# Kernel optimization log

Measured on AMD Instinct MI355X. Metric: run time of the kernel, lower is better.

The kernel has to match this reference:

```python
import jax, jax.numpy as jnp
from jax import lax
import numpy as np

B, T, E, H, ENC, V = 64, 49, 512, 512, 1024, 32000


def setup_inputs() -> dict:
    key = jax.random.key(0)
    ks = jax.random.split(key, 12)
    embeddings = jax.random.normal(ks[0], (B, T, E), jnp.float32)
    encoder_out = jax.random.normal(ks[1], (B, ENC), jnp.float32)
    # caption lengths sorted descending (module assumes this for ragged truncation)
    lens = jax.random.randint(ks[2], (B,), 10, T + 2)
    caption_lengths = jnp.sort(lens)[::-1]
    caption_lengths = caption_lengths.at[0].set(T + 1)  # max decode length == T
    s = 1.0 / np.sqrt(H)
    u = lambda k, shp, lim: jax.random.uniform(k, shp, jnp.float32, -lim, lim)
    W_ih = u(ks[3], (4 * H, E), s)
    W_hh = u(ks[4], (4 * H, H), s)
    b_ih = u(ks[5], (4 * H,), s)
    b_hh = u(ks[6], (4 * H,), s)
    se = 1.0 / np.sqrt(ENC)
    W_init_h = u(ks[7], (H, ENC), se)
    b_init_h = u(ks[8], (H,), se)
    W_init_c = u(ks[9], (H, ENC), se)
    b_init_c = u(ks[10], (H,), se)
    W_fc = u(ks[11], (V, H), 0.1)  # init_weights: uniform(-0.1, 0.1)
    b_fc = jnp.zeros((V,), jnp.float32)
    return dict(embeddings=embeddings, encoder_out=encoder_out,
                caption_lengths=caption_lengths,
                W_ih=W_ih, W_hh=W_hh, b_ih=b_ih, b_hh=b_hh,
                W_init_h=W_init_h, b_init_h=b_init_h,
                W_init_c=W_init_c, b_init_c=b_init_c,
                W_fc=W_fc, b_fc=b_fc)


def reference(embeddings, encoder_out, caption_lengths,
              W_ih, W_hh, b_ih, b_hh,
              W_init_h, b_init_h, W_init_c, b_init_c,
              W_fc, b_fc):
    # dropout is treated as identity (eval mode) for the deterministic reference
    h0 = encoder_out @ W_init_h.T + b_init_h  # [B, H]
    c0 = encoder_out @ W_init_c.T + b_init_c
    decode_lengths = caption_lengths - 1
    Tn = embeddings.shape[1]
    # mask[t, b] = True iff example b is still active at step t
    mask = jnp.arange(Tn)[:, None] < decode_lengths[None, :]  # [T, B]
    xs = jnp.transpose(embeddings, (1, 0, 2))  # [T, B, E]

    def step(carry, inp):
        h, c = carry
        x, m = inp
        gates = x @ W_ih.T + b_ih + h @ W_hh.T + b_hh  # [B, 4H]
        i, f, g, o = jnp.split(gates, 4, axis=-1)
        i = jax.nn.sigmoid(i); f = jax.nn.sigmoid(f)
        g = jnp.tanh(g); o = jax.nn.sigmoid(o)
        c_new = f * c + i * g
        h_new = o * jnp.tanh(c_new)
        preds = h_new @ W_fc.T + b_fc  # [B, V]
        m2 = m[:, None]
        # inactive rows: state frozen (torch only updates h[:batch_size_t]),
        # predictions stay zero
        h = jnp.where(m2, h_new, h)
        c = jnp.where(m2, c_new, c)
        preds = jnp.where(m2, preds, 0.0)
        return (h, c), preds

    (_, _), preds = lax.scan(step, (h0, c0), (xs, mask))
    predictions = jnp.transpose(preds, (1, 0, 2))  # [B, T, V]
    return predictions, decode_lengths
```

## Files before the change

### kernel.cpp

```cpp
#include <hip/hip_runtime.h>
#include <stdint.h>

#define B_    64
#define T_    49
#define E_    512
#define H_    512
#define ENC_  1024
#define V_    32000
#define G4_   2048
#define M_    3136
#define MPAD_ 3200
#define NPROD 32
#define NWG   512
#define NTN   250

typedef __attribute__((ext_vector_type(8))) short bf16x8;
typedef __attribute__((ext_vector_type(4))) float f32x4;

static __device__ __forceinline__ unsigned short f2bf(float f) {
  union { float f; uint32_t u; } v; v.f = f;
  uint32_t r = v.u + 0x7FFFu + ((v.u >> 16) & 1u);
  return (unsigned short)(r >> 16);
}

static __device__ __forceinline__ void async16(const void* g, void* lds) {
  __builtin_amdgcn_global_load_lds(
      (const __attribute__((address_space(1))) unsigned int*)g,
      (__attribute__((address_space(3))) unsigned int*)lds, 16, 0, 0);
}

static __device__ __forceinline__ float sigf(float x) { return 1.0f / (1.0f + expf(-x)); }

__global__ __launch_bounds__(256) void convert_kernel(
    const float* __restrict__ Wih, const float* __restrict__ Whh,
    const float* __restrict__ Wfc, const float* __restrict__ emb,
    unsigned short* __restrict__ WihB, unsigned short* __restrict__ WhhB,
    unsigned short* __restrict__ WfcB, unsigned short* __restrict__ AxB) {
  const int n_wih = (G4_ * E_) / 4;
  const int n_whh = (G4_ * H_) / 4;
  const int n_wfc = (V_ * H_) / 4;
  const int n_emb = (B_ * T_ * E_) / 4;
  const int n_pad = ((MPAD_ - M_) * E_) / 4;
  const long total = (long)n_wih + n_whh + n_wfc + n_emb + n_pad;
  for (long u = (long)blockIdx.x * blockDim.x + threadIdx.x; u < total;
       u += (long)gridDim.x * blockDim.x) {
    long i = u;
    if (i < n_wih) {
      float4 v = ((const float4*)Wih)[i];
      ushort4 o; o.x = f2bf(v.x); o.y = f2bf(v.y); o.z = f2bf(v.z); o.w = f2bf(v.w);
      ((ushort4*)WihB)[i] = o; continue;
    }
    i -= n_wih;
    if (i < n_whh) {
      float4 v = ((const float4*)Whh)[i];
      ushort4 o; o.x = f2bf(v.x); o.y = f2bf(v.y); o.z = f2bf(v.z); o.w = f2bf(v.w);
      ((ushort4*)WhhB)[i] = o; continue;
    }
    i -= n_whh;
    if (i < n_wfc) {
      float4 v = ((const float4*)Wfc)[i];
      ushort4 o; o.x = f2bf(v.x); o.y = f2bf(v.y); o.z = f2bf(v.z); o.w = f2bf(v.w);
      ((ushort4*)WfcB)[i] = o; continue;
    }
    i -= n_wfc;
    if (i < n_emb) {
      int bt = (int)(i >> 7);
      int e4 = (int)(i & 127);
      int b = bt / T_, t = bt - b * T_;
      float4 v = ((const float4*)emb)[i];
      ushort4 o; o.x = f2bf(v.x); o.y = f2bf(v.y); o.z = f2bf(v.z); o.w = f2bf(v.w);
      ((ushort4*)AxB)[((long)(t * 64 + b) << 7) + e4] = o; continue;
    }
    i -= n_emb;
    ushort4 z; z.x = z.y = z.z = z.w = 0;
    ((ushort4*)AxB)[((long)M_ << 7) + i] = z;
  }
}

__global__ __launch_bounds__(256) void init_kernel(
    const float* __restrict__ enc, const int* __restrict__ cap,
    const float* __restrict__ Wh, const float* __restrict__ bh,
    const float* __restrict__ Wc, const float* __restrict__ bc,
    unsigned short* __restrict__ h0b, float* __restrict__ c0,
    float* __restrict__ out_dl, int* __restrict__ meta,
    int* __restrict__ rowmap, int* __restrict__ zrowmap) {
  __shared__ __align__(16) float e[ENC_];
  __shared__ int s_nb[T_];
  __shared__ int s_start[T_ + 1];
  const int b = blockIdx.x, q = blockIdx.y, tid = threadIdx.x;
  ((float4*)e)[tid] = ((const float4*)(enc + (size_t)b * ENC_))[tid];
  __syncthreads();
  const bool is_c = tid >= 128;
  const int j = q * 128 + (tid & 127);
  const float* W = is_c ? Wc : Wh;
  float s = is_c ? bc[j] : bh[j];
  const float4* wr = (const float4*)(W + (size_t)j * ENC_);
  const float4* e4 = (const float4*)e;
#pragma unroll 4
  for (int k = 0; k < ENC_ / 4; ++k) {
    float4 w = wr[k], v = e4[k];
    s += w.x * v.x + w.y * v.y + w.z * v.z + w.w * v.w;
  }
  if (is_c) c0[(size_t)b * H_ + j] = s;
  else      h0b[(size_t)b * H_ + j] = f2bf(s);
  if (b == 0 && q == 0 && tid < B_) out_dl[tid] = (float)(cap[tid] - 1);

  if (b == 0 && q == 0) {
    __syncthreads();
    if (tid < T_) {
      int cnt = 0;
      for (int bb = 0; bb < B_; ++bb) cnt += (cap[bb] - 1 > tid) ? 1 : 0;
      s_nb[tid] = cnt;
    }
    __syncthreads();
    if (tid == 0) {
      int acc = 0;
      for (int t = 0; t < T_; ++t) { s_start[t] = acc; acc += s_nb[t]; }
      s_start[T_] = acc;
      const int Mc = acc;
      const int MT = (Mc + 127) >> 7;
      meta[100] = Mc;
      meta[101] = MT;
      meta[102] = MT * NTN;
      meta[103] = M_ - Mc;
      meta[104] = M_ - Mc;
      meta[105] = (M_ - Mc) + MT * NTN;
      for (int i = Mc; i < MT * 128; ++i) rowmap[i] = -1;
    }
    __syncthreads();
    if (tid < T_) {
      meta[tid] = s_start[tid];
      const int st = s_start[tid], nb = s_nb[tid];
      for (int bb = 0; bb < nb; ++bb) rowmap[st + bb] = bb * T_ + tid;
      int zst = 0;
      for (int t2 = 0; t2 < tid; ++t2) zst += B_ - s_nb[t2];
      for (int bb = nb; bb < B_; ++bb) zrowmap[zst + (bb - nb)] = bb * T_ + tid;
    }
    __syncthreads();
    if (tid < 26) {
      const int Mc = s_start[T_];
      const int MT = (Mc + 127) >> 7;
      if (tid < MT) {
        int last = tid * 128 + 127;
        if (last > Mc - 1) last = Mc - 1;
        int tlast = 0;
        for (int t2 = 0; t2 < T_; ++t2) if (s_start[t2] <= last) tlast = t2;
        meta[110 + tid] = tlast + 1;
      }
    }
  }
}

__global__ __launch_bounds__(256) void pad_kernel(const int* __restrict__ meta,
                                                  unsigned short* __restrict__ Hall) {
  const int Mc = meta[100], MT = meta[101];
  const int tot = (MT * 128 - Mc) * 64;
  for (int i = blockIdx.x * blockDim.x + threadIdx.x; i < tot;
       i += gridDim.x * blockDim.x) {
    const int row = Mc + (i >> 6), c = i & 63;
    ushort4 z; z.x = z.y = z.z = z.w = 0;
    *(ushort4*)((char*)Hall + (size_t)row * 1024 + c * 16) = z;
  }
}

__global__ __launch_bounds__(256) void gemm_gx(
    const unsigned short* __restrict__ A, const unsigned short* __restrict__ Bm,
    float* __restrict__ C, const float* __restrict__ bias0, const float* __restrict__ bias1) {
  __shared__ __align__(16) char smem[65536];
  const int tid = threadIdx.x, lane = tid & 63, wid = tid >> 6;
  const int nt = blockIdx.x, mt = blockIdx.y;
  const int wr = wid >> 1, wc = wid & 1;
  const int m0 = mt * 128, n0 = nt * 128;
  f32x4 acc[4][4] = {};

  auto stage = [&](int buf, int kit) {
    const int k0b = kit * 128;
#pragma unroll
    for (int i = 0; i < 4; ++i) {
      int chunk = wid * 4 + i;
      int d = chunk * 1024 + lane * 16;
      int row = d >> 7, colb = d & 127;
      int sc = colb ^ ((row & 7) << 4);
      async16((const char*)A + (size_t)(m0 + row) * 1024 + k0b + sc,
              smem + buf * 16384 + chunk * 1024);
      async16((const char*)Bm + (size_t)(n0 + row) * 1024 + k0b + sc,
              smem + 32768 + buf * 16384 + chunk * 1024);
    }
  };

  stage(0, 0);
  __syncthreads();
  for (int kit = 0; kit < 8; ++kit) {
    const int buf = kit & 1;
    if (kit < 7) stage(buf ^ 1, kit + 1);
    const char* Ab = smem + buf * 16384;
    const char* Bb = smem + 32768 + buf * 16384;
#pragma unroll
    for (int kb = 0; kb < 2; ++kb) {
      const int colb = kb * 64 + (lane >> 4) * 16;
      bf16x8 af[4], bfb[4];
#pragma unroll
      for (int rt = 0; rt < 4; ++rt) {
        int ar = wr * 64 + rt * 16 + (lane & 15);
        af[rt] = *(const bf16x8*)(Ab + ar * 128 + (colb ^ ((ar & 7) << 4)));
        int br = wc * 64 + rt * 16 + (lane & 15);
        bfb[rt] = *(const bf16x8*)(Bb + br * 128 + (colb ^ ((br & 7) << 4)));
      }
#pragma unroll
      for (int i = 0; i < 4; ++i)
#pragma unroll
        for (int j = 0; j < 4; ++j)
          acc[i][j] = __builtin_amdgcn_mfma_f32_16x16x32_bf16(af[i], bfb[j], acc[i][j], 0, 0, 0);
    }
    __syncthreads();
  }
#pragma unroll
  for (int i = 0; i < 4; ++i) {
    const int rbase = m0 + wr * 64 + i * 16 + (lane >> 4) * 4;
#pragma unroll
    for (int j = 0; j < 4; ++j) {
      const int col = n0 + wc * 64 + j * 16 + (lane & 15);
#pragma unroll
      for (int r = 0; r < 4; ++r)
        C[(size_t)(rbase + r) * G4_ + col] = acc[i][j][r] + bias0[col] + bias1[col];
    }
  }
}

__global__ __launch_bounds__(256) void fused_kernel(
    const float* __restrict__ Gx, const unsigned short* __restrict__ WhhB,
    const unsigned short* __restrict__ h0b, const float* __restrict__ c0,
    unsigned short* __restrict__ hsl, unsigned short* __restrict__ Hall,
    const unsigned short* __restrict__ WfcB, const float* __restrict__ bfc,
    const int* __restrict__ cap, float* __restrict__ outp,
    int* __restrict__ ctrl, const int* __restrict__ meta,
    const int* __restrict__ rowmap, const int* __restrict__ zrowmap) {
  __shared__ __align__(16) char smem[81920];
  const int tid = threadIdx.x, lane = tid & 63, g = tid >> 6;
  int* s_tile = (int*)(smem + 81916);

  if (blockIdx.x < NPROD) {
    __builtin_amdgcn_s_setprio(1);
    const int w = blockIdx.x, hc0 = w * 16;
    const int gcol = g * 512 + hc0 + (lane & 15);
    const int ko = (lane >> 4) * 8;
    bf16x8 wf[16];
#pragma unroll
    for (int kb = 0; kb < 16; ++kb)
      wf[kb] = *(const bf16x8*)&WhhB[(size_t)gcol * 512 + kb * 32 + ko];
    const int b = tid >> 2, hq = (tid & 3) * 4, hc = hc0 + hq;
    const int dl = cap[b] - 1;
    f32x4 creg = *(const f32x4*)&c0[b * H_ + hc];
    ushort4 hold = *(const ushort4*)&h0b[b * H_ + hc];
    const int myoff = ((b * 32) ^ (((b >> 2) & 7) << 4) ^ ((hq >> 3) << 4)) + ((hq & 7) * 2);
    {
      union { ushort4 s; unsigned long long u; } cv; cv.s = hold;
      __hip_atomic_store((unsigned long long*)((char*)hsl + w * 2048 + myoff), cv.u,
                         __ATOMIC_RELAXED, __HIP_MEMORY_SCOPE_AGENT);
    }
    int arb[4];
#pragma unroll
    for (int rt = 0; rt < 4; ++rt) {
      int ar = rt * 16 + (lane & 15);
      arb[rt] = (ar * 32) ^ (((ar >> 2) & 7) << 4) ^ (((lane >> 4) & 1) << 4);
    }
    const int chunk_hi = lane >> 5;
    float (*gl)[64][16] = (float (*)[64][16])(smem + 65536);
    asm volatile("s_waitcnt vmcnt(0)" ::: "memory");
    __syncthreads();
    if (tid == 0)
      __hip_atomic_store(&ctrl[w * 16], 1, __ATOMIC_RELAXED, __HIP_MEMORY_SCOPE_AGENT);

    for (int t = 0; t < T_; ++t) {
      const size_t gxr = ((size_t)t * 64 + b) * (size_t)G4_ + hc;
      f32x4 xi = *(const f32x4*)&Gx[gxr + 0];
      f32x4 xf = *(const f32x4*)&Gx[gxr + 512];
      f32x4 xg = *(const f32x4*)&Gx[gxr + 1024];
      f32x4 xo = *(const f32x4*)&Gx[gxr + 1536];
      __builtin_amdgcn_sched_barrier(0);
      if (tid < 64) {
        const int need = t + 1;
        for (;;) {
          int v = (lane < NPROD)
                      ? __hip_atomic_load(&ctrl[lane * 16], __ATOMIC_RELAXED, __HIP_MEMORY_SCOPE_AGENT)
                      : need;
          if (__all(v >= need)) break;
          __builtin_amdgcn_s_sleep(1);
        }
        if (tid == 0 && w == 0 && t > 0)
          __hip_atomic_store(&ctrl[512], t, __ATOMIC_RELAXED, __HIP_MEMORY_SCOPE_AGENT);
      }
      __syncthreads();
      {
        const char* src = (const char*)hsl + (t & 1) * 65536 + g * 16384 + lane * 8;
        char* dst = smem + g * 16384 + lane * 8;
        unsigned long long hv[32];
#pragma unroll
        for (int i = 0; i < 32; ++i)
          hv[i] = __hip_atomic_load((const unsigned long long*)(src + i * 512),
                                    __ATOMIC_RELAXED, __HIP_MEMORY_SCOPE_AGENT);
#pragma unroll
        for (int i = 0; i < 32; ++i)
          *(unsigned long long*)(dst + i * 512) = hv[i];
      }
      __syncthreads();
      f32x4 accp[4] = {};
#pragma unroll
      for (int kb = 0; kb < 16; ++kb) {
        const int cbase = (kb * 2 + chunk_hi) * 2048;
#pragma unroll
        for (int rt = 0; rt < 4; ++rt) {
          bf16x8 af = *(const bf16x8*)(smem + cbase + arb[rt]);
          accp[rt] = __builtin_amdgcn_mfma_f32_16x16x32_bf16(af, wf[kb], accp[rt], 0, 0, 0);
        }
      }
#pragma unroll
      for (int rt = 0; rt < 4; ++rt)
#pragma unroll
        for (int r = 0; r < 4; ++r)
          gl[g][rt * 16 + (lane >> 4) * 4 + r][lane & 15] = accp[rt][r];
      __syncthreads();
      f32x4 vi = xi + *(const f32x4*)&gl[0][b][hq];
      f32x4 vf = xf + *(const f32x4*)&gl[1][b][hq];
      f32x4 vg = xg + *(const f32x4*)&gl[2][b][hq];
      f32x4 vo = xo + *(const f32x4*)&gl[3][b][hq];
      f32x4 cn;
      ushort4 hb16;
      {
        float hv[4];
#pragma unroll
        for (int k = 0; k < 4; ++k) {
          float iv = sigf(vi[k]), fv = sigf(vf[k]), gv = tanhf(vg[k]), ov = sigf(vo[k]);
          cn[k] = fv * creg[k] + iv * gv;
          hv[k] = ov * tanhf(cn[k]);
        }
        hb16.x = f2bf(hv[0]); hb16.y = f2bf(hv[1]); hb16.z = f2bf(hv[2]); hb16.w = f2bf(hv[3]);
      }
      if (t < dl) {
        union { ushort4 s; unsigned long long u; } cv; cv.s = hb16;
        __hip_atomic_store((unsigned long long*)&Hall[((size_t)(meta[t] + b)) * H_ + hc],
                           cv.u, __ATOMIC_RELAXED, __HIP_MEMORY_SCOPE_AGENT);
        hold = hb16; creg = cn;
      }
      if (t + 1 < T_) {
        union { ushort4 s; unsigned long long u; } cv; cv.s = hold;
        __hip_atomic_store(
            (unsigned long long*)((char*)hsl + ((t + 1) & 1) * 65536 + w * 2048 + myoff),
            cv.u, __ATOMIC_RELAXED, __HIP_MEMORY_SCOPE_AGENT);
      }
      asm volatile("s_waitcnt vmcnt(0)" ::: "memory");
      __syncthreads();
      if (tid == 0)
        __hip_atomic_store(&ctrl[w * 16], t + 2, __ATOMIC_RELAXED, __HIP_MEMORY_SCOPE_AGENT);
    }
    if (w == 0 && tid < 64) {
      const int need = T_ + 1;
      for (;;) {
        int v = (lane < NPROD)
                    ? __hip_atomic_load(&ctrl[lane * 16], __ATOMIC_RELAXED, __HIP_MEMORY_SCOPE_AGENT)
                    : need;
        if (__all(v >= need)) break;
        __builtin_amdgcn_s_sleep(1);
      }
      if (tid == 0)
        __hip_atomic_store(&ctrl[512], T_, __ATOMIC_RELAXED, __HIP_MEMORY_SCOPE_AGENT);
    }
    __builtin_amdgcn_s_setprio(0);
  }

  const int NZI = meta[104];
  const int NTOT = meta[105];
  const int wid = tid >> 6;
  const int wr = wid >> 1, wc = wid & 1;
  for (;;) {
    __syncthreads();
    if (tid == 0)
      *s_tile = __hip_atomic_fetch_add(&ctrl[528], 1, __ATOMIC_RELAXED, __HIP_MEMORY_SCOPE_AGENT);
    __syncthreads();
    const int tile = *s_tile;
    if (tile >= NTOT) break;

    if (tile < NZI) {
      const int bt = zrowmap[tile];
      f32x4* dst = (f32x4*)(outp + (size_t)bt * V_);
      f32x4 z = {0.0f, 0.0f, 0.0f, 0.0f};
      for (int i = tid; i < V_ / 4; i += 256) dst[i] = z;
      continue;
    }

    const int gt = tile - NZI;
    const int mt = gt / NTN, nt = gt - mt * NTN;
    const int m0 = mt * 128, n0 = nt * 128;
    const int need = meta[110 + mt];
    if (tid == 0) {
      while (__hip_atomic_load(&ctrl[512], __ATOMIC_RELAXED, __HIP_MEMORY_SCOPE_AGENT) < need)
        __builtin_amdgcn_s_sleep(8);
    }
    __syncthreads();

    f32x4 acc[4][4] = {};
    auto stage = [&](int buf, int kit) {
      const int k0b = kit * 128;
#pragma unroll
      for (int i = 0; i < 4; ++i) {
        int chunk = wid * 4 + i;
        int d = chunk * 1024 + lane * 16;
        int row = d >> 7, colb = d & 127;
        int sc = colb ^ ((row & 7) << 4);
        async16((const char*)Hall + (size_t)(m0 + row) * 1024 + k0b + sc,
                smem + buf * 16384 + chunk * 1024);
        async16((const char*)WfcB + (size_t)(n0 + row) * 1024 + k0b + sc,
                smem + 32768 + buf * 16384 + chunk * 1024);
      }
    };
    stage(0, 0);
    __syncthreads();
    for (int kit = 0; kit < 8; ++kit) {
      const int buf = kit & 1;
      if (kit < 7) stage(buf ^ 1, kit + 1);
      const char* Ab = smem + buf * 16384;
      const char* Bb = smem + 32768 + buf * 16384;
#pragma unroll
      for (int kb = 0; kb < 2; ++kb) {
        const int colb = kb * 64 + (lane >> 4) * 16;
        bf16x8 af[4], bfb[4];
#pragma unroll
        for (int rt = 0; rt < 4; ++rt) {
          int ar = wr * 64 + rt * 16 + (lane & 15);
          af[rt] = *(const bf16x8*)(Ab + ar * 128 + (colb ^ ((ar & 7) << 4)));
          int br = wc * 64 + rt * 16 + (lane & 15);
          bfb[rt] = *(const bf16x8*)(Bb + br * 128 + (colb ^ ((br & 7) << 4)));
        }
#pragma unroll
        for (int i = 0; i < 4; ++i)
#pragma unroll
          for (int j = 0; j < 4; ++j)
            acc[i][j] = __builtin_amdgcn_mfma_f32_16x16x32_bf16(af[i], bfb[j], acc[i][j], 0, 0, 0);
      }
      __syncthreads();
    }
    float* Ct = (float*)smem;
#pragma unroll
    for (int j = 0; j < 4; ++j) {
      const int colL = wc * 64 + j * 16 + (lane & 15);
      const float bz = bfc[n0 + colL];
#pragma unroll
      for (int i = 0; i < 4; ++i) {
        const int rb = wr * 64 + i * 16 + (lane >> 4) * 4;
#pragma unroll
        for (int r = 0; r < 4; ++r) {
          const int row = rb + r;
          Ct[row * 128 + (colL ^ ((row & 7) << 2))] = acc[i][j][r] + bz;
        }
      }
    }
    __syncthreads();
    const int c4 = tid & 31;
    const int rsub = tid >> 5;
#pragma unroll
    for (int itr = 0; itr < 16; ++itr) {
      const int row = itr * 8 + rsub;
      const int bt = rowmap[m0 + row];
      if (bt < 0) continue;
      f32x4 v = *(const f32x4*)&Ct[row * 128 + ((c4 ^ (row & 7)) << 2)];
      *(f32x4*)(outp + (size_t)bt * V_ + n0 + (c4 << 2)) = v;
    }
  }
}

extern "C" void kernel_launch(void* const* d_in, const int* in_sizes, int n_in,
                              void* d_out, int out_size, void* d_ws, size_t ws_size,
                              hipStream_t stream) {
  const float* emb = (const float*)d_in[0];
  const float* enc = (const float*)d_in[1];
  const int*   cap = (const int*)d_in[2];
  const float* Wih = (const float*)d_in[3];
  const float* Whh = (const float*)d_in[4];
  const float* bih = (const float*)d_in[5];
  const float* bhh = (const float*)d_in[6];
  const float* Wh0 = (const float*)d_in[7];
  const float* bh0 = (const float*)d_in[8];
  const float* Wc0 = (const float*)d_in[9];
  const float* bc0 = (const float*)d_in[10];
  const float* Wfc = (const float*)d_in[11];
  const float* bfc = (const float*)d_in[12];
  float* out = (float*)d_out;

  char* ws = (char*)d_ws;
  size_t o = 0;
  auto carve = [&](size_t bytes) { void* p = ws + o; o += (bytes + 255) & ~(size_t)255; return p; };
  unsigned short* WihB = (unsigned short*)carve((size_t)G4_ * E_ * 2);
  unsigned short* WhhB = (unsigned short*)carve((size_t)G4_ * H_ * 2);
  unsigned short* WfcB = (unsigned short*)carve((size_t)V_ * H_ * 2);
  unsigned short* AxB  = (unsigned short*)carve((size_t)MPAD_ * E_ * 2);
  float*          Gx   = (float*)carve((size_t)MPAD_ * G4_ * 4);
  unsigned short* Hall = (unsigned short*)carve((size_t)MPAD_ * H_ * 2);
  unsigned short* h0b  = (unsigned short*)carve((size_t)B_ * H_ * 2);
  float*          cst  = (float*)carve((size_t)B_ * H_ * 4);
  unsigned short* hsl  = (unsigned short*)carve((size_t)2 * 65536);
  int*            ctrl = (int*)carve(4096);
  int*            meta = (int*)carve(1024);
  int*            rowmap = (int*)carve((size_t)MPAD_ * 4);
  int*            zrowmap = (int*)carve((size_t)MPAD_ * 4);
  (void)ws_size; (void)in_sizes; (void)n_in; (void)out_size;

  hipMemsetAsync(ctrl, 0, 4096, stream);
  convert_kernel<<<dim3(2048), dim3(256), 0, stream>>>(Wih, Whh, Wfc, emb, WihB, WhhB, WfcB, AxB);
  init_kernel<<<dim3(64, 4), dim3(256), 0, stream>>>(enc, cap, Wh0, bh0, Wc0, bc0, h0b, cst,
                                                     out + (size_t)B_ * T_ * V_,
                                                     meta, rowmap, zrowmap);
  pad_kernel<<<dim3(32), dim3(256), 0, stream>>>(meta, Hall);
  gemm_gx<<<dim3(G4_ / 128, MPAD_ / 128), dim3(256), 0, stream>>>(AxB, WihB, Gx, bih, bhh);
  fused_kernel<<<dim3(NWG), dim3(256), 0, stream>>>(Gx, WhhB, h0b, cst, hsl, Hall,
                                                    WfcB, bfc, cap, out, ctrl,
                                                    meta, rowmap, zrowmap);
}
```

Before: 467.7 us.

## Move W_fc bf16 conversion into fused kernel consumer tiles, overlapping the recurrence

The conversion of the large output-projection weight to bf16 moves out of the standalone convert kernel and becomes the first work tiles of the fused kernel's dynamic tile queue. Consumer workgroups convert it while the producer workgroups run the LSTM recurrence, and a new counter gates the projection GEMM tiles until every conversion tile has finished. Shared memory is cut by reusing the GEMM staging region for the producer's gate buffer, which needs an extra barrier per timestep in the producer loop. The aim is to hide the conversion cost behind the serial recurrence, at the risk of slowing the latency-critical producers and adding a dependency wait.

```diff
diff --git a/kernel.cpp b/kernel.cpp
--- a/kernel.cpp
+++ b/kernel.cpp
@@ -33,15 +33,14 @@
 
 __global__ __launch_bounds__(256) void convert_kernel(
     const float* __restrict__ Wih, const float* __restrict__ Whh,
-    const float* __restrict__ Wfc, const float* __restrict__ emb,
+    const float* __restrict__ emb,
     unsigned short* __restrict__ WihB, unsigned short* __restrict__ WhhB,
-    unsigned short* __restrict__ WfcB, unsigned short* __restrict__ AxB) {
+    unsigned short* __restrict__ AxB) {
   const int n_wih = (G4_ * E_) / 4;
   const int n_whh = (G4_ * H_) / 4;
-  const int n_wfc = (V_ * H_) / 4;
   const int n_emb = (B_ * T_ * E_) / 4;
   const int n_pad = ((MPAD_ - M_) * E_) / 4;
-  const long total = (long)n_wih + n_whh + n_wfc + n_emb + n_pad;
+  const long total = (long)n_wih + n_whh + n_emb + n_pad;
   for (long u = (long)blockIdx.x * blockDim.x + threadIdx.x; u < total;
        u += (long)gridDim.x * blockDim.x) {
     long i = u;
@@ -57,12 +56,6 @@
       ((ushort4*)WhhB)[i] = o; continue;
     }
     i -= n_whh;
-    if (i < n_wfc) {
-      float4 v = ((const float4*)Wfc)[i];
-      ushort4 o; o.x = f2bf(v.x); o.y = f2bf(v.y); o.z = f2bf(v.z); o.w = f2bf(v.w);
-      ((ushort4*)WfcB)[i] = o; continue;
-    }
-    i -= n_wfc;
     if (i < n_emb) {
       int bt = (int)(i >> 7);
       int e4 = (int)(i & 127);
@@ -121,10 +114,8 @@
       const int MT = (Mc + 127) >> 7;
       meta[100] = Mc;
       meta[101] = MT;
-      meta[102] = MT * NTN;
-      meta[103] = M_ - Mc;
       meta[104] = M_ - Mc;
-      meta[105] = (M_ - Mc) + MT * NTN;
+      meta[105] = NTN + (M_ - Mc) + MT * NTN;
       for (int i = Mc; i < MT * 128; ++i) rowmap[i] = -1;
     }
     __syncthreads();
@@ -231,13 +222,13 @@
     const float* __restrict__ Gx, const unsigned short* __restrict__ WhhB,
     const unsigned short* __restrict__ h0b, const float* __restrict__ c0,
     unsigned short* __restrict__ hsl, unsigned short* __restrict__ Hall,
-    const unsigned short* __restrict__ WfcB, const float* __restrict__ bfc,
-    const int* __restrict__ cap, float* __restrict__ outp,
-    int* __restrict__ ctrl, const int* __restrict__ meta,
+    const float* __restrict__ Wfc, unsigned short* __restrict__ WfcB,
+    const float* __restrict__ bfc, const int* __restrict__ cap,
+    float* __restrict__ outp, int* __restrict__ ctrl, const int* __restrict__ meta,
     const int* __restrict__ rowmap, const int* __restrict__ zrowmap) {
-  __shared__ __align__(16) char smem[81920];
+  __shared__ __align__(16) char smem[66560];
   const int tid = threadIdx.x, lane = tid & 63, g = tid >> 6;
-  int* s_tile = (int*)(smem + 81916);
+  int* s_tile = (int*)(smem + 66552);
 
   if (blockIdx.x < NPROD) {
     __builtin_amdgcn_s_setprio(1);
@@ -265,7 +256,7 @@
       arb[rt] = (ar * 32) ^ (((ar >> 2) & 7) << 4) ^ (((lane >> 4) & 1) << 4);
     }
     const int chunk_hi = lane >> 5;
-    float (*gl)[64][16] = (float (*)[64][16])(smem + 65536);
+    float (*gl)[64][16] = (float (*)[64][16])smem;
     asm volatile("s_waitcnt vmcnt(0)" ::: "memory");
     __syncthreads();
     if (tid == 0)
@@ -314,6 +305,7 @@
           accp[rt] = __builtin_amdgcn_mfma_f32_16x16x32_bf16(af, wf[kb], accp[rt], 0, 0, 0);
         }
       }
+      __syncthreads();
 #pragma unroll
       for (int rt = 0; rt < 4; ++rt)
 #pragma unroll
@@ -380,19 +372,37 @@
     const int tile = *s_tile;
     if (tile >= NTOT) break;
 
-    if (tile < NZI) {
-      const int bt = zrowmap[tile];
+    if (tile < NTN) {
+      const float4* src = (const float4*)(Wfc + (size_t)tile * 128 * 512);
+      unsigned long long* dst = (unsigned long long*)WfcB + (size_t)tile * 16384;
+      for (int i = tid; i < 16384; i += 256) {
+        float4 v = src[i];
+        union { ushort4 s; unsigned long long u; } cv;
+        cv.s.x = f2bf(v.x); cv.s.y = f2bf(v.y); cv.s.z = f2bf(v.z); cv.s.w = f2bf(v.w);
+        __hip_atomic_store(&dst[i], cv.u, __ATOMIC_RELAXED, __HIP_MEMORY_SCOPE_AGENT);
+      }
+      asm volatile("s_waitcnt vmcnt(0)" ::: "memory");
+      __syncthreads();
+      if (tid == 0)
+        __hip_atomic_fetch_add(&ctrl[544], 1, __ATOMIC_RELAXED, __HIP_MEMORY_SCOPE_AGENT);
+      continue;
+    }
+
+    if (tile < NTN + NZI) {
+      const int bt = zrowmap[tile - NTN];
       f32x4* dst = (f32x4*)(outp + (size_t)bt * V_);
       f32x4 z = {0.0f, 0.0f, 0.0f, 0.0f};
       for (int i = tid; i < V_ / 4; i += 256) dst[i] = z;
       continue;
     }
 
-    const int gt = tile - NZI;
+    const int gt = tile - NTN - NZI;
     const int mt = gt / NTN, nt = gt - mt * NTN;
     const int m0 = mt * 128, n0 = nt * 128;
     const int need = meta[110 + mt];
     if (tid == 0) {
+      while (__hip_atomic_load(&ctrl[544], __ATOMIC_RELAXED, __HIP_MEMORY_SCOPE_AGENT) < NTN)
+        __builtin_amdgcn_s_sleep(2);
       while (__hip_atomic_load(&ctrl[512], __ATOMIC_RELAXED, __HIP_MEMORY_SCOPE_AGENT) < need)
         __builtin_amdgcn_s_sleep(8);
     }
@@ -505,13 +515,13 @@
   (void)ws_size; (void)in_sizes; (void)n_in; (void)out_size;
 
   hipMemsetAsync(ctrl, 0, 4096, stream);
-  convert_kernel<<<dim3(2048), dim3(256), 0, stream>>>(Wih, Whh, Wfc, emb, WihB, WhhB, WfcB, AxB);
+  convert_kernel<<<dim3(1024), dim3(256), 0, stream>>>(Wih, Whh, emb, WihB, WhhB, AxB);
   init_kernel<<<dim3(64, 4), dim3(256), 0, stream>>>(enc, cap, Wh0, bh0, Wc0, bc0, h0b, cst,
                                                      out + (size_t)B_ * T_ * V_,
                                                      meta, rowmap, zrowmap);
   pad_kernel<<<dim3(32), dim3(256), 0, stream>>>(meta, Hall);
   gemm_gx<<<dim3(G4_ / 128, MPAD_ / 128), dim3(256), 0, stream>>>(AxB, WihB, Gx, bih, bhh);
   fused_kernel<<<dim3(NWG), dim3(256), 0, stream>>>(Gx, WhhB, h0b, cst, hsl, Hall,
-                                                    WfcB, bfc, cap, out, ctrl,
+                                                    Wfc, WfcB, bfc, cap, out, ctrl,
                                                     meta, rowmap, zrowmap);
 }
```

Measured after the change: 400.5 us. -14.4%, faster.
